# Performance work log

Measured on AMD Instinct MI355X. Metric: run time of the kernel, lower is better.

Reference implementation:

```python
import jax, jax.numpy as jnp
import numpy as np

S, P, SAMPLE_K = 512, 512, 10          # superpoints, points per superpoint, FPS samples
NUM_MASKS, H, W = 128, 512, 512
RADIUS, MASK_THRES, SIM_THRES, N_MASK, TOP_K = 0.2, 0.2, 0.5, 5, 10
FEAT_DIM = 32


def setup_inputs() -> dict:
    key = jax.random.key(0)
    k1, k2, k3, k4, k5, k6 = jax.random.split(key, 6)
    N = S * P
    pcds = jax.random.normal(k1, (N, 3), jnp.float32) * 2.0
    spt_labels = (jnp.arange(N) // P).astype(jnp.int32)  # sorted, contiguous superpoints
    masks = jax.random.bernoulli(k2, 0.15, (NUM_MASKS, H, W))
    yx = jax.random.randint(k3, (N, 2), 0, H).astype(jnp.int32)
    vis = jax.random.randint(k4, (N, 1), 0, 2).astype(jnp.int32)
    mapping = jnp.concatenate([jnp.zeros((N, 1), jnp.int32), yx, vis], axis=1)
    sam_scores = jax.random.uniform(k5, (NUM_MASKS,), jnp.float32)
    point_feas = jax.random.normal(k6, (N, FEAT_DIM), jnp.float32)
    return {"pcds": pcds, "spt_labels": spt_labels, "masks": masks,
            "mapping": mapping, "sam_scores": sam_scores, "point_feas": point_feas}


def _fps(pts, k):
    # pts: (P,3). Deterministic first index 0 (torch uses a random first index).
    d0 = jnp.linalg.norm(pts - pts[0], axis=1)
    def step(dist, _):
        idx = jnp.argmax(dist)
        dist = jnp.minimum(dist, jnp.linalg.norm(pts - pts[idx], axis=1))
        return dist, idx
    _, idxs = jax.lax.scan(step, d0, None, length=k - 1)
    return jnp.concatenate([jnp.zeros((1,), idxs.dtype), idxs])


def reference(pcds, spt_labels, masks, mapping, sam_scores, point_feas):
    # ---- FPS representatives per superpoint (all superpoints have P>=min_points) ----
    pts_g = pcds.reshape(S, P, 3)
    idxs = jax.vmap(lambda p: _fps(p, SAMPLE_K))(pts_g)              # (S, k)
    reps = jnp.take_along_axis(pts_g, idxs[:, :, None], axis=1)      # (S, k, 3)

    # ---- pairwise min distance between superpoint rep sets -> radius adjacency ----
    flat = reps.reshape(S * SAMPLE_K, 3)
    sq = jnp.sum(flat * flat, axis=1)
    D2 = sq[:, None] + sq[None, :] - 2.0 * (flat @ flat.T)           # (S*k, S*k)
    D2 = D2.reshape(S, SAMPLE_K, S, SAMPLE_K).min(axis=(1, 3))       # (S, S)
    dmin = jnp.sqrt(jnp.maximum(D2, 1e-12))
    eye = jnp.eye(S, dtype=bool)
    adjacency = jnp.where((dmin < RADIUS) & (~eye), jnp.exp(-dmin), 0.0)

    # ---- per-point mask coverage (visible points only) ----
    y = jnp.clip(mapping[:, 1], 0, H - 1)
    x = jnp.clip(mapping[:, 2], 0, W - 1)
    vis = mapping[:, 3] == 1
    coverage = masks[:, y, x].T & vis[:, None]                       # (N, num_masks)

    # ---- aggregate coverage per superpoint, keep top_k superpoints per mask ----
    counts = coverage.reshape(S, P, NUM_MASKS).sum(axis=1)
    fraction = counts.astype(jnp.float32) / (P + 1e-6)               # (S, num_masks)
    _, top_inds = jax.lax.top_k(fraction.T, TOP_K)                   # (num_masks, top_k)
    topk_mask = jnp.zeros((NUM_MASKS, S), bool).at[
        jnp.arange(NUM_MASKS)[:, None], top_inds].set(True).T        # (S, num_masks)
    frac_kept = jnp.where(topk_mask, fraction, 0.0)
    contrib = frac_kept >= MASK_THRES                                # (S, num_masks) bool

    # ---- superpoint features (mean, L2-normalized) ----
    feats = point_feas.reshape(S, P, -1).sum(axis=1) / (P + 1e-6)
    feats = feats / jnp.maximum(jnp.linalg.norm(feats, axis=1, keepdims=True), 1e-12)

    # ---- modulate adjacency by top-n_mask mask-overlap IoU and feature similarity ----
    union = contrib[:, None, :] | contrib[None, :, :]                # (S, S, num_masks)
    _, u_inds = jax.lax.top_k(union.astype(jnp.float32), N_MASK)     # (S, S, n_mask)
    mi = jnp.take_along_axis(jnp.broadcast_to(contrib[:, None, :], union.shape), u_inds, axis=2)
    mj = jnp.take_along_axis(jnp.broadcast_to(contrib[None, :, :], union.shape), u_inds, axis=2)
    inter = (mi & mj).sum(-1).astype(jnp.float32)
    uni = (mi | mj).sum(-1).astype(jnp.float32)
    overlap = inter / (uni + 1e-6)
    sim = jnp.clip((feats @ feats.T + 1.0) / 2.0, 0.0, 1.0)
    sim = jnp.where(sim < SIM_THRES, 1.0, sim)
    mod = overlap * sim
    adjacency = jnp.where(adjacency > 0, jnp.maximum(mod, adjacency), adjacency)

    # ---- superpoint confidence scores ----
    weights = frac_kept * sam_scores[None, :]
    conf = jnp.maximum(weights.sum(1) / (frac_kept.sum(1) + 1e-6), 0.0)
    return adjacency, conf
```

## Files before the change

### kernel.cpp

```cpp
#include <hip/hip_runtime.h>
#include <cstddef>
#include <cstdint>

#define SPTS 512
#define PPS  512
#define KFPS 10
#define NMSK 128
#define HH 512
#define WW 512
#define HWPIX (HH*WW)
#define FDIM 32
#define TOPK_SEL 10
#define NMASK_TOP 5

__device__ __forceinline__ unsigned mask_val(const void* raw, long long idx, int mode) {
    if (mode == 0) return ((const unsigned char*)raw)[idx] ? 1u : 0u;
    if (mode == 1) return ((const int*)raw)[idx] ? 1u : 0u;
    return (((const float*)raw)[idx] != 0.0f) ? 1u : 0u;
}

__device__ __forceinline__ int detect_mode(const void* raw) {
    __shared__ int s_any1, s_any23;
    if (threadIdx.x == 0) { s_any1 = 0; s_any23 = 0; }
    __syncthreads();
    if (threadIdx.x < 256) {
        uint4 w = ((const uint4*)raw)[threadIdx.x];
        unsigned b1  = (w.x >> 8 | w.y >> 8 | w.z >> 8 | w.w >> 8) & 0xFFu;
        unsigned b23 = ((w.x >> 16) | (w.y >> 16) | (w.z >> 16) | (w.w >> 16)) & 0xFFFFu;
        if (b1)  atomicOr(&s_any1, 1);
        if (b23) atomicOr(&s_any23, 1);
    }
    __syncthreads();
    return s_any1 ? 0 : (s_any23 ? 2 : 1);
}

__device__ __forceinline__ void fps_wave(const float* pcds, float* reps, int s, int lane) {
    const float* base = pcds + (size_t)s * PPS * 3;
    float px_[8], py_[8], pz_[8];
#pragma unroll
    for (int k = 0; k < 8; ++k) {
        int p = lane + 64 * k;
        px_[k] = base[p * 3 + 0];
        py_[k] = base[p * 3 + 1];
        pz_[k] = base[p * 3 + 2];
    }
    float ax = __shfl(px_[0], 0), ay = __shfl(py_[0], 0), az = __shfl(pz_[0], 0);
    float dist[8];
#pragma unroll
    for (int k = 0; k < 8; ++k) {
        float dx = px_[k] - ax, dy = py_[k] - ay, dz = pz_[k] - az;
        dist[k] = sqrtf(dx * dx + dy * dy + dz * dz);
    }
    if (lane == 0) {
        reps[((size_t)s * KFPS + 0) * 3 + 0] = ax;
        reps[((size_t)s * KFPS + 0) * 3 + 1] = ay;
        reps[((size_t)s * KFPS + 0) * 3 + 2] = az;
    }
    for (int kk = 1; kk < KFPS; ++kk) {
        float bv = dist[0]; int bk = 0;
#pragma unroll
        for (int k = 1; k < 8; ++k)
            if (dist[k] > bv) { bv = dist[k]; bk = k; }
        float v = bv; int pidx = lane + 64 * bk;
#pragma unroll
        for (int off = 1; off < 64; off <<= 1) {
            float ov = __shfl_xor(v, off);
            int   op = __shfl_xor(pidx, off);
            if (ov > v || (ov == v && op < pidx)) { v = ov; pidx = op; }
        }
        int owner = pidx & 63, slot = pidx >> 6;
        float sx = px_[0], sy = py_[0], sz = pz_[0];
#pragma unroll
        for (int j = 1; j < 8; ++j)
            if (slot == j) { sx = px_[j]; sy = py_[j]; sz = pz_[j]; }
        sx = __shfl(sx, owner); sy = __shfl(sy, owner); sz = __shfl(sz, owner);
        if (lane == 0) {
            reps[((size_t)s * KFPS + kk) * 3 + 0] = sx;
            reps[((size_t)s * KFPS + kk) * 3 + 1] = sy;
            reps[((size_t)s * KFPS + kk) * 3 + 2] = sz;
        }
#pragma unroll
        for (int k = 0; k < 8; ++k) {
            float dx = px_[k] - sx, dy = py_[k] - sy, dz = pz_[k] - sz;
            float d = sqrtf(dx * dx + dy * dy + dz * dz);
            dist[k] = fminf(dist[k], d);
        }
    }
}

__global__ void __launch_bounds__(256) k_repack_fps(const void* raw, unsigned* maskbits,
                                                    const float* pcds, float* reps) {
    int bid = blockIdx.x;
    int t = threadIdx.x;
    if (bid < 2048) {
        int mode = detect_mode(raw);
        if (mode == 0) {
            if (bid >= 1024) return;
            int quarter = bid & 3;
            int ptile   = bid >> 2;
            int pix0 = ptile * 1024 + t * 4;
            const unsigned char* base = (const unsigned char*)raw + (size_t)quarter * 32 * HWPIX + pix0;
            unsigned w[4] = {0, 0, 0, 0};
#pragma unroll
            for (int m = 0; m < 32; ++m) {
                unsigned v = *(const unsigned*)(base + (size_t)m * HWPIX);
#pragma unroll
                for (int p = 0; p < 4; ++p)
                    w[p] |= ((v >> (8 * p)) & 1u) << m;
            }
#pragma unroll
            for (int p = 0; p < 4; ++p)
                maskbits[(size_t)(pix0 + p) * 4 + quarter] = w[p];
        } else {
            int gtid = bid * 256 + t;
            int pix  = gtid & (HWPIX - 1);
            int half = gtid >> 18;
            const unsigned* base = (const unsigned*)raw + (size_t)half * 64 * HWPIX + pix;
            unsigned w0 = 0, w1 = 0;
#pragma unroll
            for (int m = 0; m < 32; ++m)
                w0 |= (unsigned)(base[(size_t)m * HWPIX] != 0u) << m;
#pragma unroll
            for (int m = 0; m < 32; ++m)
                w1 |= (unsigned)(base[(size_t)(m + 32) * HWPIX] != 0u) << m;
            uint2 o; o.x = w0; o.y = w1;
            *(uint2*)(maskbits + (size_t)pix * 4 + half * 2) = o;
        }
        return;
    }
    fps_wave(pcds, reps, (bid - 2048) * 4 + (t >> 6), t & 63);
}

__global__ void __launch_bounds__(PPS) k_counts_feats(const int* mapping, const unsigned* maskbits,
                                                      const void* raw, int packed,
                                                      const float* feas,
                                                      int* counts, unsigned* contrib, float* feats) {
    int s = blockIdx.x;
    int t = threadIdx.x;
    if (t < 4) contrib[s * 4 + t] = 0u;
    __shared__ int cnt[NMSK];
    __shared__ float fpart[16][FDIM];
    if (t < NMSK) cnt[t] = 0;
    int mode = 0;
    if (!packed) mode = detect_mode(raw);
    __syncthreads();
    int i = s * PPS + t;
    int4 mp = ((const int4*)mapping)[i];
    int y = min(max(mp.y, 0), HH - 1);
    int x = min(max(mp.z, 0), WW - 1);
    bool vis = (mp.w == 1);
    unsigned w0 = 0, w1 = 0, w2 = 0, w3 = 0;
    if (vis) {
        if (packed) {
            uint4 v = *((const uint4*)(maskbits + (size_t)(y * WW + x) * 4));
            w0 = v.x; w1 = v.y; w2 = v.z; w3 = v.w;
        } else {
            long long pix = (long long)y * WW + x;
            for (int m = 0; m < NMSK; ++m) {
                unsigned v = mask_val(raw, (long long)m * HWPIX + pix, mode);
                if (m < 32)       w0 |= v << m;
                else if (m < 64)  w1 |= v << (m - 32);
                else if (m < 96)  w2 |= v << (m - 64);
                else              w3 |= v << (m - 96);
            }
        }
    }
    int lane = t & 63;
    unsigned ww[4] = { w0, w1, w2, w3 };
#pragma unroll
    for (int m = 0; m < NMSK; ++m) {
        unsigned bit = (ww[m >> 5] >> (m & 31)) & 1u;
        unsigned long long bal = __ballot((int)bit);
        if (lane == 0) atomicAdd(&cnt[m], (int)__popcll(bal));
    }
    {
        int g = t >> 5, d = t & 31;
        const float* fb = feas + (size_t)s * PPS * FDIM;
        float acc = 0.0f;
#pragma unroll 8
        for (int it = 0; it < 32; ++it) acc += fb[(g + 16 * it) * FDIM + d];
        fpart[g][d] = acc;
    }
    __syncthreads();
    if (t < NMSK) counts[s * NMSK + t] = cnt[t];
    if (t < FDIM) {
        float sum = 0.0f;
#pragma unroll
        for (int q = 0; q < 16; ++q) sum += fpart[q][t];
        float f = sum / 512.0f;
        float sq = f * f;
#pragma unroll
        for (int off = 16; off >= 1; off >>= 1) sq += __shfl_xor(sq, off);
        feats[s * FDIM + t] = f / fmaxf(sqrtf(sq), 1e-12f);
    }
}

__global__ void __launch_bounds__(SPTS) k_topk(const int* counts, unsigned* contrib, float* frac_kept) {
    int m = blockIdx.x;
    int s = threadIdx.x;
    __shared__ int cl[SPTS];
    cl[s] = counts[s * NMSK + m];
    __syncthreads();
    int c = cl[s];
    int rank = 0;
    for (int s2 = 0; s2 < SPTS; ++s2) {
        int c2 = cl[s2];
        rank += (c2 > c || (c2 == c && s2 < s)) ? 1 : 0;
    }
    bool sel = (rank < TOPK_SEL);
    float frac = (float)c / 512.0f;
    frac_kept[s * NMSK + m] = sel ? frac : 0.0f;
    if (sel && frac >= 0.2f)
        atomicOr(&contrib[s * 4 + (m >> 5)], 1u << (m & 31));
}

__global__ void __launch_bounds__(256) k_adjmod(const float* reps, const unsigned* contrib,
                                                const float* feats, const float* frac_kept,
                                                const float* sam, float* out) {
    if (blockIdx.x >= (SPTS * SPTS) / 256) {
        int s = (blockIdx.x - (SPTS * SPTS) / 256) * 256 + threadIdx.x;
        if (s < SPTS) {
            float sw = 0.0f, sf = 0.0f;
            for (int m = 0; m < NMSK; ++m) {
                float fk = frac_kept[s * NMSK + m];
                sw += fk * sam[m];
                sf += fk;
            }
            out[(size_t)SPTS * SPTS + s] = fmaxf(sw / (sf + 1e-6f), 0.0f);
        }
        return;
    }
    int idx = blockIdx.x * blockDim.x + threadIdx.x;
    int i = idx >> 9, j = idx & 511;
    __shared__ float ri[KFPS * 3];
    __shared__ float sqi[KFPS];
    if (threadIdx.x < KFPS * 3) ri[threadIdx.x] = reps[(size_t)i * KFPS * 3 + threadIdx.x];
    __syncthreads();
    if (threadIdx.x < KFPS) {
        float X = ri[threadIdx.x * 3], Y = ri[threadIdx.x * 3 + 1], Z = ri[threadIdx.x * 3 + 2];
        sqi[threadIdx.x] = X * X + Y * Y + Z * Z;
    }
    __syncthreads();
    float rjx[KFPS], rjy[KFPS], rjz[KFPS], sqj[KFPS];
    const float* rp = reps + (size_t)j * KFPS * 3;
#pragma unroll
    for (int b = 0; b < KFPS; ++b) {
        float X = rp[b * 3], Y = rp[b * 3 + 1], Z = rp[b * 3 + 2];
        rjx[b] = X; rjy[b] = Y; rjz[b] = Z;
        sqj[b] = X * X + Y * Y + Z * Z;
    }
    float mn = 1e30f;
#pragma unroll
    for (int a = 0; a < KFPS; ++a) {
        float ax = ri[a * 3], ay = ri[a * 3 + 1], az = ri[a * 3 + 2];
        float sa = sqi[a];
#pragma unroll
        for (int b = 0; b < KFPS; ++b) {
            float dot = ax * rjx[b] + ay * rjy[b] + az * rjz[b];
            float d2 = (sa + sqj[b]) - 2.0f * dot;
            mn = fminf(mn, d2);
        }
    }
    float dmin = sqrtf(fmaxf(mn, 1e-12f));
    float a = (dmin < 0.2f && i != j) ? expf(-dmin) : 0.0f;
    if (a > 0.0f) {
        uint4 c4i = *((const uint4*)(contrib + (size_t)i * 4));
        uint4 c4j = *((const uint4*)(contrib + (size_t)j * 4));
        unsigned cia[4] = { c4i.x, c4i.y, c4i.z, c4i.w };
        unsigned cja[4] = { c4j.x, c4j.y, c4j.z, c4j.w };
        int taken = 0, inter = 0, uni = 0;
#pragma unroll
        for (int w = 0; w < 4; ++w) {
            unsigned u = cia[w] | cja[w];
            unsigned both = cia[w] & cja[w];
            while (u && taken < NMASK_TOP) {
                unsigned bit = u & (~u + 1u);
                uni++;
                if (both & bit) inter++;
                u ^= bit; taken++;
            }
        }
        float overlap = (float)inter / ((float)uni + 1e-6f);
        const float* fi = feats + (size_t)i * FDIM;
        const float* fj = feats + (size_t)j * FDIM;
        float dot = 0.0f;
#pragma unroll
        for (int d = 0; d < FDIM; ++d) dot += fi[d] * fj[d];
        float sim = (dot + 1.0f) / 2.0f;
        sim = fminf(fmaxf(sim, 0.0f), 1.0f);
        if (sim < 0.5f) sim = 1.0f;
        a = fmaxf(overlap * sim, a);
    }
    out[idx] = a;
}

extern "C" void kernel_launch(void* const* d_in, const int* in_sizes, int n_in,
                              void* d_out, int out_size, void* d_ws, size_t ws_size,
                              hipStream_t stream) {
    const float* pcds    = (const float*)d_in[0];
    const void*  masks   = d_in[2];
    const int*   mapping = (const int*)d_in[3];
    const float* sam     = (const float*)d_in[4];
    const float* feas    = (const float*)d_in[5];
    float* out = (float*)d_out;

    char* ws = (char*)d_ws;
    size_t off = 0;
    auto take = [&](size_t bytes) -> void* {
        void* p = ws + off;
        off += (bytes + 255) & ~(size_t)255;
        return p;
    };
    float*    reps      = (float*)take((size_t)SPTS * KFPS * 3 * sizeof(float));
    int*      counts    = (int*)take((size_t)SPTS * NMSK * sizeof(int));
    unsigned* contrib   = (unsigned*)take((size_t)SPTS * 4 * sizeof(unsigned));
    float*    frac_kept = (float*)take((size_t)SPTS * NMSK * sizeof(float));
    float*    feats     = (float*)take((size_t)SPTS * FDIM * sizeof(float));
    unsigned* maskbits  = (unsigned*)take((size_t)HWPIX * 4 * sizeof(unsigned));
    size_t need_packed = off;
    int packed = (ws_size >= need_packed) ? 1 : 0;

    k_repack_fps<<<2176, 256, 0, stream>>>(masks, maskbits, pcds, reps);
    k_counts_feats<<<SPTS, PPS, 0, stream>>>(mapping, maskbits, masks, packed, feas,
                                             counts, contrib, feats);
    k_topk<<<NMSK, SPTS, 0, stream>>>(counts, contrib, frac_kept);
    k_adjmod<<<(SPTS * SPTS) / 256 + 2, 256, 0, stream>>>(reps, contrib, feats, frac_kept, sam, out);
}
```

Before: 80.27 us.

## Repack all 128 mask bits per thread with fewer, wider blocks

The mask bit-repack now uses 256 blocks in which each thread handles 4 pixels across all 128 masks, instead of splitting masks across quarter or half blocks. It issues batches of 8 loads in flight and writes one 16-byte word per pixel, which removes partial-word stores and repeated mode detection over many blocks. The FPS block offset and grid size are adjusted to match. The cost is much less parallelism in the memory-bound repack (far fewer waves to hide latency) and more registers per thread.

Measured after the change: 70.34 us, median of 2. 12.4% less time.

```diff
diff --git a/kernel.cpp b/kernel.cpp
--- a/kernel.cpp
+++ b/kernel.cpp
@@ -92,43 +92,50 @@
                                                     const float* pcds, float* reps) {
     int bid = blockIdx.x;
     int t = threadIdx.x;
-    if (bid < 2048) {
+    if (bid < 256) {
         int mode = detect_mode(raw);
+        int pix0 = bid * 1024 + t * 4;
+        unsigned w[4][4] = {};
         if (mode == 0) {
-            if (bid >= 1024) return;
-            int quarter = bid & 3;
-            int ptile   = bid >> 2;
-            int pix0 = ptile * 1024 + t * 4;
-            const unsigned char* base = (const unsigned char*)raw + (size_t)quarter * 32 * HWPIX + pix0;
-            unsigned w[4] = {0, 0, 0, 0};
-#pragma unroll
-            for (int m = 0; m < 32; ++m) {
-                unsigned v = *(const unsigned*)(base + (size_t)m * HWPIX);
-#pragma unroll
-                for (int p = 0; p < 4; ++p)
-                    w[p] |= ((v >> (8 * p)) & 1u) << m;
-            }
-#pragma unroll
-            for (int p = 0; p < 4; ++p)
-                maskbits[(size_t)(pix0 + p) * 4 + quarter] = w[p];
+            const unsigned char* base = (const unsigned char*)raw + pix0;
+            for (int g = 0; g < 16; ++g) {
+                unsigned v[8];
+#pragma unroll
+                for (int j = 0; j < 8; ++j)
+                    v[j] = *(const unsigned*)(base + (size_t)(g * 8 + j) * HWPIX);
+#pragma unroll
+                for (int j = 0; j < 8; ++j) {
+                    int m = g * 8 + j; int q = m >> 5; unsigned sh = (unsigned)(m & 31);
+#pragma unroll
+                    for (int p = 0; p < 4; ++p)
+                        w[q][p] |= ((v[j] >> (8 * p)) & 1u) << sh;
+                }
+            }
         } else {
-            int gtid = bid * 256 + t;
-            int pix  = gtid & (HWPIX - 1);
-            int half = gtid >> 18;
-            const unsigned* base = (const unsigned*)raw + (size_t)half * 64 * HWPIX + pix;
-            unsigned w0 = 0, w1 = 0;
-#pragma unroll
-            for (int m = 0; m < 32; ++m)
-                w0 |= (unsigned)(base[(size_t)m * HWPIX] != 0u) << m;
-#pragma unroll
-            for (int m = 0; m < 32; ++m)
-                w1 |= (unsigned)(base[(size_t)(m + 32) * HWPIX] != 0u) << m;
-            uint2 o; o.x = w0; o.y = w1;
-            *(uint2*)(maskbits + (size_t)pix * 4 + half * 2) = o;
+            const unsigned* basep = (const unsigned*)raw + pix0;
+            for (int g = 0; g < 16; ++g) {
+                uint4 v[8];
+#pragma unroll
+                for (int j = 0; j < 8; ++j)
+                    v[j] = *(const uint4*)(basep + (size_t)(g * 8 + j) * HWPIX);
+#pragma unroll
+                for (int j = 0; j < 8; ++j) {
+                    int m = g * 8 + j; int q = m >> 5; unsigned sh = (unsigned)(m & 31);
+                    w[q][0] |= (unsigned)(v[j].x != 0u) << sh;
+                    w[q][1] |= (unsigned)(v[j].y != 0u) << sh;
+                    w[q][2] |= (unsigned)(v[j].z != 0u) << sh;
+                    w[q][3] |= (unsigned)(v[j].w != 0u) << sh;
+                }
+            }
+        }
+#pragma unroll
+        for (int p = 0; p < 4; ++p) {
+            uint4 o; o.x = w[0][p]; o.y = w[1][p]; o.z = w[2][p]; o.w = w[3][p];
+            *(uint4*)(maskbits + (size_t)(pix0 + p) * 4) = o;
         }
         return;
     }
-    fps_wave(pcds, reps, (bid - 2048) * 4 + (t >> 6), t & 63);
+    fps_wave(pcds, reps, (bid - 256) * 4 + (t >> 6), t & 63);
 }
 
 __global__ void __launch_bounds__(PPS) k_counts_feats(const int* mapping, const unsigned* maskbits,
@@ -320,7 +327,7 @@
     size_t need_packed = off;
     int packed = (ws_size >= need_packed) ? 1 : 0;
 
-    k_repack_fps<<<2176, 256, 0, stream>>>(masks, maskbits, pcds, reps);
+    k_repack_fps<<<384, 256, 0, stream>>>(masks, maskbits, pcds, reps);
     k_counts_feats<<<SPTS, PPS, 0, stream>>>(mapping, maskbits, masks, packed, feas,
                                              counts, contrib, feats);
     k_topk<<<NMSK, SPTS, 0, stream>>>(counts, contrib, frac_kept);
```
